# Performance work log

Hardware: AMD Instinct MI355X
Metric: run time of the kernel (lower is better)

The kernel has to match this reference:

```python
import jax, jax.numpy as jnp
import numpy as np

NP, P = 5, 5  # number of body parts, joints per part


def _windows(t):
    # (binf, length) for the 6 overlapping temporal windows of sequence()
    h, th = t // 2, t // 3
    return [(0, t), (0, h), (h, t - h), (0, th), (th, th), (2 * th, t - 2 * th)]


def _block(xw):
    # xw: (B, NP, P, L, C) -> Gaussian-embedding blocks (B, NP, L, C+1, C+1)
    B, n, p, L, C = xw.shape
    # smoothing over the P (joint-within-part) axis, as in the original code
    xs = xw.at[:, :, 1:-1].set((xw[:, :, 1:-1] + xw[:, :, :-2] + xw[:, :, 2:]) / 3)
    mu = xs.mean(axis=2)  # (B, NP, L, C)
    # temporally shifted centered slices (shifts over the L axis)
    x0 = xw - mu[:, :, None]                       # (B, NP, P, L, C)
    xm = xw[:, :, :, :-2] - mu[:, :, None, 1:-1]   # (B, NP, P, L-2, C)
    xp = xw[:, :, :, 2:] - mu[:, :, None, 1:-1]    # (B, NP, P, L-2, C)
    outer_mean = lambda a: jnp.einsum('bnptc,bnptd->bntcd', a, a) / p
    cov_mid = (outer_mean(xm) + outer_mean(x0[:, :, :, 1:-1]) + outer_mean(xp)) / 3
    xb = x0[:, :, :, ::L - 1]  # boundary frames 0 and L-1
    cov_b = jnp.einsum('bnptc,bnptd->bntcd', xb, xb) / p
    cov = jnp.zeros((B, n, L, C, C), xw.dtype)
    cov = cov.at[:, :, 1:-1].set(cov_mid)
    cov = cov.at[:, :, ::L - 1].set(cov_b)
    elt00 = cov + mu[..., :, None] * mu[..., None, :]  # cov + mu mu^T
    top = jnp.concatenate([elt00, mu[..., None]], axis=-1)            # (.., C, C+1)
    ones = jnp.ones((B, n, L, 1, 1), xw.dtype)
    bot = jnp.concatenate([mu[..., None, :], ones], axis=-1)          # (.., 1, C+1)
    return jnp.concatenate([top, bot], axis=-2)                        # (.., C+1, C+1)


def setup_inputs() -> dict:
    key = jax.random.key(0)
    x = jax.random.normal(key, (256, 600, 25, 3, 1), dtype=jnp.float32)
    return {"input": x}


def reference(input):
    B, T, J, C, _ = input.shape
    # (B, T, J, C, 1) -> (B, NP, P, T, C)  (matches transpose(1,2).reshape)
    x = jnp.moveaxis(input[..., 0], 1, 2).reshape(B, NP, P, T, C)
    blocks = [_block(x[:, :, :, b:b + L]) for b, L in _windows(T)]
    return jnp.concatenate(blocks, axis=2)  # (B, NP, sum(L_s), C+1, C+1)
```

## Files before the change

### kernel.cpp

```cpp
#include <hip/hip_runtime.h>


#define T_ 600
#define CH_ 100
#define NCH_ 6

typedef float fx4 __attribute__((ext_vector_type(4)));

#define BAR_LDS() do { asm volatile("s_waitcnt lgkmcnt(0)" ::: "memory"); \
                       __builtin_amdgcn_s_barrier(); } while (0)

__global__ __launch_bounds__(256) void gauss_agg_kernel(const float* __restrict__ x,
                                                        float* __restrict__ out) {
    __shared__ float raw[7650];
    __shared__ float4 obuf[256 * 5];

    int blk = blockIdx.x;
    int ch  = blk % NCH_;
    int b   = blk / NCH_;
    int tc  = ch * CH_;
    int tid = (int)threadIdx.x;

    const float4* srcv = reinterpret_cast<const float4*>(x + ((size_t)b * T_ + tc) * 75);
    float4* rawv = reinterpret_cast<float4*>(raw);
    #pragma unroll
    for (int i = 0; i < 8; ++i) {
        int e = i * 256 + tid;
        if (e < 1875) rawv[e] = srcv[e];
    }
    if (tid < 150) {
        int rp  = (tid < 75) ? (tc > 0 ? tc - 1 : 0)
                             : (tc + 100 < T_ ? tc + 100 : T_ - 1);
        int col = (tid < 75) ? tid : tid - 75;
        raw[7500 + tid] = x[((size_t)b * T_ + rp) * 75 + col];
    }
    BAR_LDS();

    const float w5[5] = {4.f, 2.f, 3.f, 2.f, 4.f};
    fx4* outf4 = reinterpret_cast<fx4*>(out);

    for (int m = 0; m < 6; ++m) {
        int s = m * 256 + tid;
        if (s < 1500) {
            int n  = s / 300;
            int q  = s - n * 300;
            int w  = q / 100;
            int tl = q - w * 100;
            int tt = tc + tl;

            bool boundary;
            if (w == 0)      boundary = (tt == 0) || (tt == 599);
            else if (w == 1) boundary = (tt == 0) || (tt == 299) || (tt == 300) || (tt == 599);
            else             boundary = (tt == 0) || (tt == 199) || (tt == 200) ||
                                        (tt == 399) || (tt == 400) || (tt == 599);

            int midoff = tl * 75 + n * 15;
            const float* rc = &raw[midoff];

            float s0=0.f,s1=0.f,s2=0.f, m0=0.f,m1=0.f,m2=0.f;
            float A00=0.f,A01=0.f,A02=0.f,A11=0.f,A12=0.f,A22=0.f;
            #pragma unroll
            for (int p = 0; p < 5; ++p) {
                float a = rc[p*3+0], c = rc[p*3+1], d = rc[p*3+2];
                s0 += a; s1 += c; s2 += d;
                m0 += w5[p]*a; m1 += w5[p]*c; m2 += w5[p]*d;
                A00 += a*a; A01 += a*c; A02 += a*d;
                A11 += c*c; A12 += c*d; A22 += d*d;
            }
            float mu0 = m0*(1.f/15.f), mu1 = m1*(1.f/15.f), mu2 = m2*(1.f/15.f);

            float inv = 0.2f;
            if (!boundary) {
                const float* rp_ = &raw[(tl == 0)  ? 7500 + n * 15 : midoff - 75];
                const float* rn_ = &raw[(tl == 99) ? 7575 + n * 15 : midoff + 75];
                #pragma unroll
                for (int dstep = 0; dstep < 2; ++dstep) {
                    const float* rn = dstep ? rn_ : rp_;
                    #pragma unroll
                    for (int p = 0; p < 5; ++p) {
                        float a = rn[p*3+0], c = rn[p*3+1], d = rn[p*3+2];
                        s0 += a; s1 += c; s2 += d;
                        A00 += a*a; A01 += a*c; A02 += a*d;
                        A11 += c*c; A12 += c*d; A22 += d*d;
                    }
                }
                inv = 1.f/15.f;
            }

            float mb0 = s0*inv, mb1 = s1*inv, mb2 = s2*inv;
            float e00 = A00*inv - 2.f*mu0*mb0 + 2.f*mu0*mu0;
            float e01 = A01*inv - mu0*mb1 - mb0*mu1 + 2.f*mu0*mu1;
            float e02 = A02*inv - mu0*mb2 - mb0*mu2 + 2.f*mu0*mu2;
            float e11 = A11*inv - 2.f*mu1*mb1 + 2.f*mu1*mu1;
            float e12 = A12*inv - mu1*mb2 - mb1*mu2 + 2.f*mu1*mu2;
            float e22 = A22*inv - 2.f*mu2*mb2 + 2.f*mu2*mu2;

            int base = tid * 5;
            obuf[base + 0] = make_float4(e00, e01, e02, mu0);
            obuf[base + 1] = make_float4(e01, e11, e12, mu1);
            obuf[base + 2] = make_float4(e02, e12, e22, mu2);
            obuf[base + 3] = make_float4(mu0, mu1, mu2, 1.f);
        }
        BAR_LDS();

        int nslots  = (1500 - m * 256 < 256) ? (1500 - m * 256) : 256;
        int npieces = nslots * 4;
        #pragma unroll
        for (int k = 0; k < 4; ++k) {
            int f = k * 256 + tid;
            if (f < npieces) {
                int sl = f >> 2, pc = f & 3;
                int s2 = m * 256 + sl;
                int n  = s2 / 300;
                int q  = s2 - n * 300;
                int w  = q / 100;
                int tl = q - w * 100;
                int tt = tc + tl;
                size_t o = ((size_t)(b * 5 + n) * 1800 + w * 600 + tt) * 4 + pc;
                float4 v = obuf[sl * 5 + pc];
                fx4 nv; nv.x = v.x; nv.y = v.y; nv.z = v.z; nv.w = v.w;
                __builtin_nontemporal_store(nv, &outf4[o]);
            }
        }
        BAR_LDS();
    }
}

extern "C" void kernel_launch(void* const* d_in, const int* in_sizes, int n_in,
                              void* d_out, int out_size, void* d_ws, size_t ws_size,
                              hipStream_t stream) {
    const float* x = (const float*)d_in[0];
    float* out = (float*)d_out;
    gauss_agg_kernel<<<256 * NCH_, 256, 0, stream>>>(x, out);
}
```

Baseline: 40.19 us.

## Deduplicate window computations and halve time chunk per block

Each time step's per-part statistics are now computed once per block (250 interior slots plus 5 slots for the one boundary frame a chunk can contain) and reused across the three window output copies, instead of recomputing 1500 slots across 6 compute/store rounds. Chunks shrink to 50 frames with 12 blocks per batch, the halo rows are loaded contiguously with aligned float4 copies, and the per-round barriers collapse into a single compute phase followed by one store phase. This cuts redundant arithmetic and barriers and doubles block count, at the cost of some index logic for mapping outputs to shared slots.

```diff
diff --git a/kernel.cpp b/kernel.cpp
--- a/kernel.cpp
+++ b/kernel.cpp
@@ -2,8 +2,8 @@
 
 
 #define T_ 600
-#define CH_ 100
-#define NCH_ 6
+#define CH_ 50
+#define NCH_ 12
 
 typedef float fx4 __attribute__((ext_vector_type(4)));
 
@@ -12,7 +12,7 @@
 
 __global__ __launch_bounds__(256) void gauss_agg_kernel(const float* __restrict__ x,
                                                         float* __restrict__ out) {
-    __shared__ float raw[7650];
+    __shared__ float raw[3908];
     __shared__ float4 obuf[256 * 5];
 
     int blk = blockIdx.x;
@@ -21,108 +21,124 @@
     int tc  = ch * CH_;
     int tid = (int)threadIdx.x;
 
-    const float4* srcv = reinterpret_cast<const float4*>(x + ((size_t)b * T_ + tc) * 75);
-    float4* rawv = reinterpret_cast<float4*>(raw);
-    #pragma unroll
-    for (int i = 0; i < 8; ++i) {
-        int e = i * 256 + tid;
-        if (e < 1875) rawv[e] = srcv[e];
+    int vtt = -1;
+    switch (ch) {
+        case 0:  vtt = 0;   break;
+        case 3:  vtt = 199; break;
+        case 4:  vtt = 200; break;
+        case 5:  vtt = 299; break;
+        case 6:  vtt = 300; break;
+        case 7:  vtt = 399; break;
+        case 8:  vtt = 400; break;
+        case 11: vtt = 599; break;
+        default: break;
     }
-    if (tid < 150) {
-        int rp  = (tid < 75) ? (tc > 0 ? tc - 1 : 0)
-                             : (tc + 100 < T_ ? tc + 100 : T_ - 1);
-        int col = (tid < 75) ? tid : tid - 75;
-        raw[7500 + tid] = x[((size_t)b * T_ + rp) * 75 + col];
+
+    int start = (tc == 0) ? 0 : tc - 1;
+    int end   = tc + CH_ + 1; if (end > T_) end = T_;
+    int nrows = end - start;
+    int ofs   = tc - start;
+    int tot   = nrows * 75;
+    size_t gbase = (size_t)b * 45000 + (size_t)start * 75;
+
+    int head = (int)((4 - (gbase & 3)) & 3);
+    int off  = (4 - head) & 3;
+    {
+        if (head > tot) head = tot;
+        int nv   = (tot - head) >> 2;
+        int tail = tot - head - nv * 4;
+        if (tid < head) raw[off + tid] = x[gbase + tid];
+        const float4* srcv = reinterpret_cast<const float4*>(x + gbase + head);
+        float4* rawv = reinterpret_cast<float4*>(&raw[off + head]);
+        #pragma unroll
+        for (int i = 0; i < 4; ++i) {
+            int e = i * 256 + tid;
+            if (e < nv) rawv[e] = srcv[e];
+        }
+        if (tid < tail) raw[off + head + 4 * nv + tid] = x[gbase + head + 4 * nv + tid];
     }
     BAR_LDS();
 
-    const float w5[5] = {4.f, 2.f, 3.f, 2.f, 4.f};
+    {
+        bool isvar = (tid >= 250);
+        int n, tt;
+        if (!isvar) { n = tid / 50; tt = tc + (tid - n * 50); }
+        else        { int k = tid - 250; n = (k > 4) ? 4 : k; tt = (vtt < 0) ? tc : vtt; }
+        int li = tt - tc + ofs;
+        int lp = li - 1; if (lp < 0) lp = 0;
+        int ln = li + 1;
+
+        const float w5[5] = {4.f, 2.f, 3.f, 2.f, 4.f};
+        const float* rc = &raw[off + li * 75 + n * 15];
+
+        float s0=0.f,s1=0.f,s2=0.f, m0=0.f,m1=0.f,m2=0.f;
+        float A00=0.f,A01=0.f,A02=0.f,A11=0.f,A12=0.f,A22=0.f;
+        #pragma unroll
+        for (int p = 0; p < 5; ++p) {
+            float a = rc[p*3+0], c = rc[p*3+1], d = rc[p*3+2];
+            s0 += a; s1 += c; s2 += d;
+            m0 += w5[p]*a; m1 += w5[p]*c; m2 += w5[p]*d;
+            A00 += a*a; A01 += a*c; A02 += a*d;
+            A11 += c*c; A12 += c*d; A22 += d*d;
+        }
+        float mu0 = m0*(1.f/15.f), mu1 = m1*(1.f/15.f), mu2 = m2*(1.f/15.f);
+
+        float inv = 0.2f;
+        if (!isvar) {
+            const float* r0 = &raw[off + lp * 75 + n * 15];
+            const float* r1 = &raw[off + ln * 75 + n * 15];
+            #pragma unroll
+            for (int dstep = 0; dstep < 2; ++dstep) {
+                const float* rn = dstep ? r1 : r0;
+                #pragma unroll
+                for (int p = 0; p < 5; ++p) {
+                    float a = rn[p*3+0], c = rn[p*3+1], d = rn[p*3+2];
+                    s0 += a; s1 += c; s2 += d;
+                    A00 += a*a; A01 += a*c; A02 += a*d;
+                    A11 += c*c; A12 += c*d; A22 += d*d;
+                }
+            }
+            inv = 1.f/15.f;
+        }
+
+        float mb0 = s0*inv, mb1 = s1*inv, mb2 = s2*inv;
+        float e00 = A00*inv - 2.f*mu0*mb0 + 2.f*mu0*mu0;
+        float e01 = A01*inv - mu0*mb1 - mb0*mu1 + 2.f*mu0*mu1;
+        float e02 = A02*inv - mu0*mb2 - mb0*mu2 + 2.f*mu0*mu2;
+        float e11 = A11*inv - 2.f*mu1*mb1 + 2.f*mu1*mu1;
+        float e12 = A12*inv - mu1*mb2 - mb1*mu2 + 2.f*mu1*mu2;
+        float e22 = A22*inv - 2.f*mu2*mb2 + 2.f*mu2*mu2;
+
+        int base = tid * 5;
+        obuf[base + 0] = make_float4(e00, e01, e02, mu0);
+        obuf[base + 1] = make_float4(e01, e11, e12, mu1);
+        obuf[base + 2] = make_float4(e02, e12, e22, mu2);
+        obuf[base + 3] = make_float4(mu0, mu1, mu2, 1.f);
+    }
+    BAR_LDS();
+
     fx4* outf4 = reinterpret_cast<fx4*>(out);
-
-    for (int m = 0; m < 6; ++m) {
-        int s = m * 256 + tid;
-        if (s < 1500) {
-            int n  = s / 300;
-            int q  = s - n * 300;
-            int w  = q / 100;
-            int tl = q - w * 100;
+    #pragma unroll
+    for (int k = 0; k < 12; ++k) {
+        int f = k * 256 + tid;
+        if (f < 3000) {
+            int sl = f >> 2, pc = f & 3;
+            int n  = sl / 150;
+            int q  = sl - n * 150;
+            int w  = q / 50;
+            int tl = q - w * 50;
             int tt = tc + tl;
-
-            bool boundary;
-            if (w == 0)      boundary = (tt == 0) || (tt == 599);
-            else if (w == 1) boundary = (tt == 0) || (tt == 299) || (tt == 300) || (tt == 599);
-            else             boundary = (tt == 0) || (tt == 199) || (tt == 200) ||
-                                        (tt == 399) || (tt == 400) || (tt == 599);
-
-            int midoff = tl * 75 + n * 15;
-            const float* rc = &raw[midoff];
-
-            float s0=0.f,s1=0.f,s2=0.f, m0=0.f,m1=0.f,m2=0.f;
-            float A00=0.f,A01=0.f,A02=0.f,A11=0.f,A12=0.f,A22=0.f;
-            #pragma unroll
-            for (int p = 0; p < 5; ++p) {
-                float a = rc[p*3+0], c = rc[p*3+1], d = rc[p*3+2];
-                s0 += a; s1 += c; s2 += d;
-                m0 += w5[p]*a; m1 += w5[p]*c; m2 += w5[p]*d;
-                A00 += a*a; A01 += a*c; A02 += a*d;
-                A11 += c*c; A12 += c*d; A22 += d*d;
-            }
-            float mu0 = m0*(1.f/15.f), mu1 = m1*(1.f/15.f), mu2 = m2*(1.f/15.f);
-
-            float inv = 0.2f;
-            if (!boundary) {
-                const float* rp_ = &raw[(tl == 0)  ? 7500 + n * 15 : midoff - 75];
-                const float* rn_ = &raw[(tl == 99) ? 7575 + n * 15 : midoff + 75];
-                #pragma unroll
-                for (int dstep = 0; dstep < 2; ++dstep) {
-                    const float* rn = dstep ? rn_ : rp_;
-                    #pragma unroll
-                    for (int p = 0; p < 5; ++p) {
-                        float a = rn[p*3+0], c = rn[p*3+1], d = rn[p*3+2];
-                        s0 += a; s1 += c; s2 += d;
-                        A00 += a*a; A01 += a*c; A02 += a*d;
-                        A11 += c*c; A12 += c*d; A22 += d*d;
-                    }
-                }
-                inv = 1.f/15.f;
-            }
-
-            float mb0 = s0*inv, mb1 = s1*inv, mb2 = s2*inv;
-            float e00 = A00*inv - 2.f*mu0*mb0 + 2.f*mu0*mu0;
-            float e01 = A01*inv - mu0*mb1 - mb0*mu1 + 2.f*mu0*mu1;
-            float e02 = A02*inv - mu0*mb2 - mb0*mu2 + 2.f*mu0*mu2;
-            float e11 = A11*inv - 2.f*mu1*mb1 + 2.f*mu1*mu1;
-            float e12 = A12*inv - mu1*mb2 - mb1*mu2 + 2.f*mu1*mu2;
-            float e22 = A22*inv - 2.f*mu2*mb2 + 2.f*mu2*mu2;
-
-            int base = tid * 5;
-            obuf[base + 0] = make_float4(e00, e01, e02, mu0);
-            obuf[base + 1] = make_float4(e01, e11, e12, mu1);
-            obuf[base + 2] = make_float4(e02, e12, e22, mu2);
-            obuf[base + 3] = make_float4(mu0, mu1, mu2, 1.f);
+            bool bd;
+            if (w == 0)      bd = (tt == 0) || (tt == 599);
+            else if (w == 1) { int r = tt % 300; bd = (r == 0) || (r == 299); }
+            else             { int r = tt % 200; bd = (r == 0) || (r == 199); }
+            int oi = bd ? (250 + n) : sl % 250;
+            if (!bd) oi = n * 50 + tl;
+            size_t o = ((size_t)(b * 5 + n) * 1800 + w * 600 + tt) * 4 + pc;
+            float4 v = obuf[oi * 5 + pc];
+            fx4 nv; nv.x = v.x; nv.y = v.y; nv.z = v.z; nv.w = v.w;
+            __builtin_nontemporal_store(nv, &outf4[o]);
         }
-        BAR_LDS();
-
-        int nslots  = (1500 - m * 256 < 256) ? (1500 - m * 256) : 256;
-        int npieces = nslots * 4;
-        #pragma unroll
-        for (int k = 0; k < 4; ++k) {
-            int f = k * 256 + tid;
-            if (f < npieces) {
-                int sl = f >> 2, pc = f & 3;
-                int s2 = m * 256 + sl;
-                int n  = s2 / 300;
-                int q  = s2 - n * 300;
-                int w  = q / 100;
-                int tl = q - w * 100;
-                int tt = tc + tl;
-                size_t o = ((size_t)(b * 5 + n) * 1800 + w * 600 + tt) * 4 + pc;
-                float4 v = obuf[sl * 5 + pc];
-                fx4 nv; nv.x = v.x; nv.y = v.y; nv.z = v.z; nv.w = v.w;
-                __builtin_nontemporal_store(nv, &outf4[o]);
-            }
-        }
-        BAR_LDS();
     }
 }
 
```

Result: faster. 37.89 us (-5.7%).

## Deduplicate per-frame block math across windows and use 512-thread blocks

Applied to the files above, without the earlier changes.

The three temporal windows share identical interior blocks for a given frame, so each block now computes every (part, frame) once, plus a few special boundary-frame variants per chunk. The output stage then gathers from a shared LDS table to write all three windows. This removes the threefold redundant arithmetic and the six compute/store rounds with their barriers. Block size doubles to 512 and the LDS output buffer grows, which may lower occupancy.

```diff
diff --git a/kernel.cpp b/kernel.cpp
--- a/kernel.cpp
+++ b/kernel.cpp
@@ -10,10 +10,10 @@
 #define BAR_LDS() do { asm volatile("s_waitcnt lgkmcnt(0)" ::: "memory"); \
                        __builtin_amdgcn_s_barrier(); } while (0)
 
-__global__ __launch_bounds__(256) void gauss_agg_kernel(const float* __restrict__ x,
+__global__ __launch_bounds__(512) void gauss_agg_kernel(const float* __restrict__ x,
                                                         float* __restrict__ out) {
     __shared__ float raw[7650];
-    __shared__ float4 obuf[256 * 5];
+    __shared__ float4 obuf[512 * 5];
 
     int blk = blockIdx.x;
     int ch  = blk % NCH_;
@@ -21,108 +21,116 @@
     int tc  = ch * CH_;
     int tid = (int)threadIdx.x;
 
-    const float4* srcv = reinterpret_cast<const float4*>(x + ((size_t)b * T_ + tc) * 75);
-    float4* rawv = reinterpret_cast<float4*>(raw);
-    #pragma unroll
-    for (int i = 0; i < 8; ++i) {
-        int e = i * 256 + tid;
-        if (e < 1875) rawv[e] = srcv[e];
+    int vtt1 = -1, vtt2 = -1;
+    switch (ch) {
+        case 0: vtt1 = 0;   break;
+        case 1: vtt1 = 199; break;
+        case 2: vtt1 = 200; vtt2 = 299; break;
+        case 3: vtt1 = 300; vtt2 = 399; break;
+        case 4: vtt1 = 400; break;
+        case 5: vtt1 = 599; break;
     }
-    if (tid < 150) {
-        int rp  = (tid < 75) ? (tc > 0 ? tc - 1 : 0)
-                             : (tc + 100 < T_ ? tc + 100 : T_ - 1);
-        int col = (tid < 75) ? tid : tid - 75;
-        raw[7500 + tid] = x[((size_t)b * T_ + rp) * 75 + col];
+
+    {
+        const float4* srcv = reinterpret_cast<const float4*>(x + ((size_t)b * T_ + tc) * 75);
+        float4* rawv = reinterpret_cast<float4*>(raw);
+        #pragma unroll
+        for (int i = 0; i < 4; ++i) {
+            int e = i * 512 + tid;
+            if (e < 1875) rawv[e] = srcv[e];
+        }
+        if (tid < 150) {
+            int rp  = (tid < 75) ? (tc > 0 ? tc - 1 : 0)
+                                 : (tc + CH_ < T_ ? tc + CH_ : T_ - 1);
+            int col = (tid < 75) ? tid : tid - 75;
+            raw[7500 + tid] = x[((size_t)b * T_ + rp) * 75 + col];
+        }
     }
     BAR_LDS();
 
     const float w5[5] = {4.f, 2.f, 3.f, 2.f, 4.f};
     fx4* outf4 = reinterpret_cast<fx4*>(out);
 
-    for (int m = 0; m < 6; ++m) {
-        int s = m * 256 + tid;
-        if (s < 1500) {
-            int n  = s / 300;
-            int q  = s - n * 300;
+    if (tid < 510) {
+        bool isvar = (tid >= 500);
+        int n, tt;
+        if (!isvar) { n = tid / 100; tt = tc + (tid - n * 100); }
+        else if (tid < 505) { n = tid - 500; tt = (vtt1 < 0) ? tc : vtt1; }
+        else                { n = tid - 505; tt = (vtt2 < 0) ? tc : vtt2; }
+        int tl = tt - tc;
+
+        int midoff = tl * 75 + n * 15;
+        const float* rc = &raw[midoff];
+        const float* r0 = &raw[(tl == 0)  ? 7500 + n * 15 : midoff - 75];
+        const float* r1 = &raw[(tl == 99) ? 7575 + n * 15 : midoff + 75];
+
+        float s0=0.f,s1=0.f,s2=0.f, m0=0.f,m1=0.f,m2=0.f;
+        float A00=0.f,A01=0.f,A02=0.f,A11=0.f,A12=0.f,A22=0.f;
+        #pragma unroll
+        for (int p = 0; p < 5; ++p) {
+            float a = rc[p*3+0], c = rc[p*3+1], d = rc[p*3+2];
+            s0 += a; s1 += c; s2 += d;
+            m0 += w5[p]*a; m1 += w5[p]*c; m2 += w5[p]*d;
+            A00 += a*a; A01 += a*c; A02 += a*d;
+            A11 += c*c; A12 += c*d; A22 += d*d;
+        }
+        float mu0 = m0*(1.f/15.f), mu1 = m1*(1.f/15.f), mu2 = m2*(1.f/15.f);
+
+        float inv = 0.2f;
+        if (!isvar) {
+            #pragma unroll
+            for (int dstep = 0; dstep < 2; ++dstep) {
+                const float* rn = dstep ? r1 : r0;
+                #pragma unroll
+                for (int p = 0; p < 5; ++p) {
+                    float a = rn[p*3+0], c = rn[p*3+1], d = rn[p*3+2];
+                    s0 += a; s1 += c; s2 += d;
+                    A00 += a*a; A01 += a*c; A02 += a*d;
+                    A11 += c*c; A12 += c*d; A22 += d*d;
+                }
+            }
+            inv = 1.f/15.f;
+        }
+
+        float mb0 = s0*inv, mb1 = s1*inv, mb2 = s2*inv;
+        float e00 = A00*inv - 2.f*mu0*mb0 + 2.f*mu0*mu0;
+        float e01 = A01*inv - mu0*mb1 - mb0*mu1 + 2.f*mu0*mu1;
+        float e02 = A02*inv - mu0*mb2 - mb0*mu2 + 2.f*mu0*mu2;
+        float e11 = A11*inv - 2.f*mu1*mb1 + 2.f*mu1*mu1;
+        float e12 = A12*inv - mu1*mb2 - mb1*mu2 + 2.f*mu1*mu2;
+        float e22 = A22*inv - 2.f*mu2*mb2 + 2.f*mu2*mu2;
+
+        int base = tid * 5;
+        obuf[base + 0] = make_float4(e00, e01, e02, mu0);
+        obuf[base + 1] = make_float4(e01, e11, e12, mu1);
+        obuf[base + 2] = make_float4(e02, e12, e22, mu2);
+        obuf[base + 3] = make_float4(mu0, mu1, mu2, 1.f);
+    }
+    BAR_LDS();
+
+    #pragma unroll
+    for (int k = 0; k < 12; ++k) {
+        int f = k * 512 + tid;
+        if (f < 6000) {
+            int sl = f >> 2, pc = f & 3;
+            int n  = sl / 300;
+            int q  = sl - n * 300;
             int w  = q / 100;
             int tl = q - w * 100;
             int tt = tc + tl;
-
-            bool boundary;
-            if (w == 0)      boundary = (tt == 0) || (tt == 599);
-            else if (w == 1) boundary = (tt == 0) || (tt == 299) || (tt == 300) || (tt == 599);
-            else             boundary = (tt == 0) || (tt == 199) || (tt == 200) ||
-                                        (tt == 399) || (tt == 400) || (tt == 599);
-
-            int midoff = tl * 75 + n * 15;
-            const float* rc = &raw[midoff];
-
-            float s0=0.f,s1=0.f,s2=0.f, m0=0.f,m1=0.f,m2=0.f;
-            float A00=0.f,A01=0.f,A02=0.f,A11=0.f,A12=0.f,A22=0.f;
-            #pragma unroll
-            for (int p = 0; p < 5; ++p) {
-                float a = rc[p*3+0], c = rc[p*3+1], d = rc[p*3+2];
-                s0 += a; s1 += c; s2 += d;
-                m0 += w5[p]*a; m1 += w5[p]*c; m2 += w5[p]*d;
-                A00 += a*a; A01 += a*c; A02 += a*d;
-                A11 += c*c; A12 += c*d; A22 += d*d;
-            }
-            float mu0 = m0*(1.f/15.f), mu1 = m1*(1.f/15.f), mu2 = m2*(1.f/15.f);
-
-            float inv = 0.2f;
-            if (!boundary) {
-                const float* rp_ = &raw[(tl == 0)  ? 7500 + n * 15 : midoff - 75];
-                const float* rn_ = &raw[(tl == 99) ? 7575 + n * 15 : midoff + 75];
-                #pragma unroll
-                for (int dstep = 0; dstep < 2; ++dstep) {
-                    const float* rn = dstep ? rn_ : rp_;
-                    #pragma unroll
-                    for (int p = 0; p < 5; ++p) {
-                        float a = rn[p*3+0], c = rn[p*3+1], d = rn[p*3+2];
-                        s0 += a; s1 += c; s2 += d;
-                        A00 += a*a; A01 += a*c; A02 += a*d;
-                        A11 += c*c; A12 += c*d; A22 += d*d;
-                    }
-                }
-                inv = 1.f/15.f;
-            }
-
-            float mb0 = s0*inv, mb1 = s1*inv, mb2 = s2*inv;
-            float e00 = A00*inv - 2.f*mu0*mb0 + 2.f*mu0*mu0;
-            float e01 = A01*inv - mu0*mb1 - mb0*mu1 + 2.f*mu0*mu1;
-            float e02 = A02*inv - mu0*mb2 - mb0*mu2 + 2.f*mu0*mu2;
-            float e11 = A11*inv - 2.f*mu1*mb1 + 2.f*mu1*mu1;
-            float e12 = A12*inv - mu1*mb2 - mb1*mu2 + 2.f*mu1*mu2;
-            float e22 = A22*inv - 2.f*mu2*mb2 + 2.f*mu2*mu2;
-
-            int base = tid * 5;
-            obuf[base + 0] = make_float4(e00, e01, e02, mu0);
-            obuf[base + 1] = make_float4(e01, e11, e12, mu1);
-            obuf[base + 2] = make_float4(e02, e12, e22, mu2);
-            obuf[base + 3] = make_float4(mu0, mu1, mu2, 1.f);
+            bool bd;
+            if (w == 0)      bd = (tt == 0) || (tt == 599);
+            else if (w == 1) { int r = tt % 300; bd = (r == 0) || (r == 299); }
+            else             { int r = tt % 200; bd = (r == 0) || (r == 199); }
+            int oi;
+            if (!bd)             oi = n * 100 + tl;
+            else if (tt == vtt1) oi = 500 + n;
+            else                 oi = 505 + n;
+            size_t o = ((size_t)(b * 5 + n) * 1800 + w * 600 + tt) * 4 + pc;
+            float4 v = obuf[oi * 5 + pc];
+            fx4 nv; nv.x = v.x; nv.y = v.y; nv.z = v.z; nv.w = v.w;
+            __builtin_nontemporal_store(nv, &outf4[o]);
         }
-        BAR_LDS();
-
-        int nslots  = (1500 - m * 256 < 256) ? (1500 - m * 256) : 256;
-        int npieces = nslots * 4;
-        #pragma unroll
-        for (int k = 0; k < 4; ++k) {
-            int f = k * 256 + tid;
-            if (f < npieces) {
-                int sl = f >> 2, pc = f & 3;
-                int s2 = m * 256 + sl;
-                int n  = s2 / 300;
-                int q  = s2 - n * 300;
-                int w  = q / 100;
-                int tl = q - w * 100;
-                int tt = tc + tl;
-                size_t o = ((size_t)(b * 5 + n) * 1800 + w * 600 + tt) * 4 + pc;
-                float4 v = obuf[sl * 5 + pc];
-                fx4 nv; nv.x = v.x; nv.y = v.y; nv.z = v.z; nv.w = v.w;
-                __builtin_nontemporal_store(nv, &outf4[o]);
-            }
-        }
-        BAR_LDS();
     }
 }
 
@@ -131,5 +139,5 @@
                               hipStream_t stream) {
     const float* x = (const float*)d_in[0];
     float* out = (float*)d_out;
-    gauss_agg_kernel<<<256 * NCH_, 256, 0, stream>>>(x, out);
+    gauss_agg_kernel<<<256 * NCH_, 512, 0, stream>>>(x, out);
 }
```

Measured after the change: 37.46 us. 6.8% less time.
